# Performance work log

Measured on AMD Instinct MI355X. Metric: run time of the kernel, lower is better.

Reference implementation:

```python
import jax, jax.numpy as jnp
import numpy as np

B = 2
SPATIAL = (480, 360, 32)  # cylindrical grid (rho, phi, z) as in Cylinder3D
N = 400000
C = 32
EPS = 1e-5
NEG_SLOPE = 0.01
OFFSETS = [(d0, d2) for d0 in (-1, 0, 1) for d2 in (-1, 0, 1)]  # kernel (3,1,3)


def setup_inputs() -> dict:
    key = jax.random.key(0)
    k1, k2 = jax.random.split(key)
    # unique active voxel coordinates: sample unique linear indices then decode
    total = B * SPATIAL[0] * SPATIAL[1] * SPATIAL[2]
    rng = np.random.default_rng(0)
    lin = rng.choice(total, size=N, replace=False).astype(np.int64)
    b = lin // (SPATIAL[0] * SPATIAL[1] * SPATIAL[2])
    r = lin % (SPATIAL[0] * SPATIAL[1] * SPATIAL[2])
    c0 = r // (SPATIAL[1] * SPATIAL[2])
    r = r % (SPATIAL[1] * SPATIAL[2])
    c1 = r // SPATIAL[2]
    c2 = r % SPATIAL[2]
    coords = jnp.asarray(np.stack([b, c0, c1, c2], axis=1), dtype=jnp.int32)
    features = jax.random.normal(k1, (N, C), dtype=jnp.float32)
    weight = jax.random.normal(k2, (9, C, C), dtype=jnp.float32) * (1.0 / np.sqrt(9 * C))
    gamma = jnp.ones((C,), dtype=jnp.float32)
    beta = jnp.zeros((C,), dtype=jnp.float32)
    return {"features": features, "coords": coords, "weight": weight,
            "gamma": gamma, "beta": beta}


def _subm_conv(features, coords, weight):
    n = features.shape[0]
    # dense coordinate -> row-index lookup table (rulebook hash)
    lookup = jnp.full((B,) + SPATIAL, -1, dtype=jnp.int32)
    lookup = lookup.at[coords[:, 0], coords[:, 1], coords[:, 2], coords[:, 3]].set(
        jnp.arange(n, dtype=jnp.int32))
    out = jnp.zeros((n, weight.shape[-1]), dtype=features.dtype)
    for k, (d0, d2) in enumerate(OFFSETS):
        n0 = coords[:, 1] + d0
        n2 = coords[:, 3] + d2
        valid = (n0 >= 0) & (n0 < SPATIAL[0]) & (n2 >= 0) & (n2 < SPATIAL[2])
        nbr = lookup[coords[:, 0],
                     jnp.clip(n0, 0, SPATIAL[0] - 1),
                     coords[:, 2],
                     jnp.clip(n2, 0, SPATIAL[2] - 1)]
        nbr = jnp.where(valid, nbr, -1)
        # gather (masked) -> GEMM -> accumulate (scatter to same active sites)
        gathered = jnp.where((nbr >= 0)[:, None],
                             features[jnp.clip(nbr, 0)], 0.0)
        out = out + gathered @ weight[k]
    return out


def reference(features, coords, weight, gamma, beta):
    x = _subm_conv(features, coords, weight)          # [N, C]
    x = jnp.where(x >= 0, x, NEG_SLOPE * x)           # LeakyReLU (before BN per forward)
    mean = jnp.mean(x, axis=0)                        # BatchNorm1d, training mode
    var = jnp.mean((x - mean) ** 2, axis=0)           # biased variance
    y = (x - mean) * jax.lax.rsqrt(var + EPS) * gamma + beta
    return y
```

## Files before the change

### kernel.cpp

```cpp
#include <hip/hip_runtime.h>

#define S0 480
#define S1 360
#define S2 32
#define CH 32
#define EPS 1e-5f
#define SLOPE 0.01f

#define LOOKUP_INTS (2 * S0 * S1 * S2)
#define LOOKUP_BYTES ((size_t)LOOKUP_INTS * 4)

typedef short short8 __attribute__((ext_vector_type(8)));
typedef float f32x16 __attribute__((ext_vector_type(16)));

__device__ __forceinline__ unsigned short f32_to_bf16_rne(float f) {
    union { float f; unsigned int u; } v; v.f = f;
    unsigned int x = v.u;
    unsigned int r = (x + 0x7FFFu + ((x >> 16) & 1u)) >> 16;
    return (unsigned short)r;
}

__global__ __launch_bounds__(256) void scatter_convert_k(
    const float4* __restrict__ features,
    const int4*   __restrict__ coords,
    int*          __restrict__ lookup,
    unsigned short* __restrict__ featb,
    int n)
{
    int i = blockIdx.x * 256 + threadIdx.x;
    if (i >= n) return;
    int4 c = coords[i];
    int lin = ((c.x * S0 + c.y) * S1 + c.z) * S2 + c.w;
    lookup[lin] = i;

    const float4* fr = features + (size_t)i * 8;
    ushort4* fo = (ushort4*)(featb + (size_t)i * CH);
#pragma unroll
    for (int j = 0; j < 8; ++j) {
        float4 f = fr[j];
        ushort4 u;
        u.x = f32_to_bf16_rne(f.x);
        u.y = f32_to_bf16_rne(f.y);
        u.z = f32_to_bf16_rne(f.z);
        u.w = f32_to_bf16_rne(f.w);
        fo[j] = u;
    }
}

__global__ void bfrag_prep_k(const float* __restrict__ weight,
                             short8* __restrict__ bfrag)
{
    int lane = threadIdx.x;
    int half = lane >> 5;
    int col  = lane & 31;
#pragma unroll
    for (int t = 0; t < 9; ++t)
#pragma unroll
        for (int h = 0; h < 2; ++h) {
            short8 fr;
#pragma unroll
            for (int j = 0; j < 8; ++j) {
                int ic = h * 16 + half * 8 + j;
                fr[j] = (short)f32_to_bf16_rne(weight[t * (CH * CH) + ic * CH + col]);
            }
            bfrag[(t * 2 + h) * 64 + lane] = fr;
        }
}

__global__ __launch_bounds__(256) void conv_mfma_k(
    const short*  __restrict__ featb,
    const int4*   __restrict__ coords,
    const int*    __restrict__ lookup,
    const short8* __restrict__ bfrag,
    float*        __restrict__ xout,
    float*        __restrict__ stats,
    int n, int ntile, int nwaves)
{
    int tid  = threadIdx.x;
    int lane = tid & 63;
    int wv   = tid >> 6;
    int half = lane >> 5;
    int col  = lane & 31;

    short8 B[9][2];
#pragma unroll
    for (int t = 0; t < 9; ++t)
#pragma unroll
        for (int h = 0; h < 2; ++h)
            B[t][h] = bfrag[(t * 2 + h) * 64 + lane];

    float s = 0.f, q = 0.f;

    int gw = blockIdx.x * 4 + wv;
    for (int tile = gw; tile < ntile; tile += nwaves) {
        int p = tile * 32 + col;
        int4 c = coords[p];
        int lin = ((c.x * S0 + c.y) * S1 + c.z) * S2 + c.w;
        int nbr[9];
#pragma unroll
        for (int d0 = 0; d0 < 3; ++d0) {
            int n0 = c.y + d0 - 1;
            bool v0 = (n0 >= 0) & (n0 < S0);
#pragma unroll
            for (int d2 = 0; d2 < 3; ++d2) {
                int n2 = c.w + d2 - 1;
                bool v = v0 & (n2 >= 0) & (n2 < S2);
                nbr[d0 * 3 + d2] = v ? lookup[lin + (d0 - 1) * (S1 * S2) + (d2 - 1)] : -1;
            }
        }

        f32x16 acc;
#pragma unroll
        for (int r = 0; r < 16; ++r) acc[r] = 0.f;

#pragma unroll
        for (int t = 0; t < 9; ++t) {
            int nb = nbr[t];
            short8 a0, a1;
            if (nb >= 0) {
                const short* fp = featb + (size_t)nb * CH;
                a0 = *(const short8*)(fp + half * 8);
                a1 = *(const short8*)(fp + 16 + half * 8);
            } else {
#pragma unroll
                for (int j = 0; j < 8; ++j) { a0[j] = 0; a1[j] = 0; }
            }
            acc = __builtin_amdgcn_mfma_f32_32x32x16_bf16(a0, B[t][0], acc, 0, 0, 0);
            acc = __builtin_amdgcn_mfma_f32_32x32x16_bf16(a1, B[t][1], acc, 0, 0, 0);
        }

        bool live = (p < n);
        float* xrow = xout + (size_t)tile * 32 * CH + col;
#pragma unroll
        for (int r = 0; r < 16; ++r) {
            float v = acc[r];
            v = v >= 0.f ? v : SLOPE * v;
            int row = (r & 3) + 8 * (r >> 2) + 4 * half;
            if (live) xrow[row * CH] = v;
            s += v; q += v * v;
        }
    }

    s += __shfl_xor(s, 32);
    q += __shfl_xor(q, 32);

    __shared__ float lsum[4][32];
    __shared__ float lsq[4][32];
    if (lane < 32) { lsum[wv][col] = s; lsq[wv][col] = q; }
    __syncthreads();
    if (tid < 32) {
        float S = lsum[0][tid] + lsum[1][tid] + lsum[2][tid] + lsum[3][tid];
        atomicAdd(&stats[tid], S);
    } else if (tid < 64) {
        int cc = tid - 32;
        float Q = lsq[0][cc] + lsq[1][cc] + lsq[2][cc] + lsq[3][cc];
        atomicAdd(&stats[CH + cc], Q);
    }
}

__global__ __launch_bounds__(256) void bn_apply_k(
    float* __restrict__ x,
    const float* __restrict__ stats,
    const float* __restrict__ gamma,
    const float* __restrict__ beta,
    int n)
{
    int total4 = n * (CH / 4);
    int stride = gridDim.x * blockDim.x;
    int g = blockIdx.x * blockDim.x + threadIdx.x;
    int c4 = g & 7;

    float scale[4], shift[4];
    float rn = 1.0f / (float)n;
#pragma unroll
    for (int j = 0; j < 4; ++j) {
        int oc = c4 * 4 + j;
        float m  = stats[oc] * rn;
        float v  = stats[CH + oc] * rn - m * m;
        float iv = rsqrtf(v + EPS) * gamma[oc];
        scale[j] = iv;
        shift[j] = beta[oc] - m * iv;
    }

    float4* x4 = (float4*)x;
    for (; g < total4; g += stride) {
        float4 v = x4[g];
        v.x = fmaf(v.x, scale[0], shift[0]);
        v.y = fmaf(v.y, scale[1], shift[1]);
        v.z = fmaf(v.z, scale[2], shift[2]);
        v.w = fmaf(v.w, scale[3], shift[3]);
        x4[g] = v;
    }
}

extern "C" void kernel_launch(void* const* d_in, const int* in_sizes, int n_in,
                              void* d_out, int out_size, void* d_ws, size_t ws_size,
                              hipStream_t stream)
{
    const float* features = (const float*)d_in[0];
    const int4*  coords   = (const int4*)d_in[1];
    const float* weight   = (const float*)d_in[2];
    const float* gamma    = (const float*)d_in[3];
    const float* beta     = (const float*)d_in[4];
    float* out = (float*)d_out;

    int n = in_sizes[0] / CH;
    int ntile = (n + 31) / 32;

    unsigned short* featb = (unsigned short*)d_ws;
    size_t featb_bytes = (size_t)n * CH * 2;
    featb_bytes = (featb_bytes + 255) & ~(size_t)255;
    int* lookup = (int*)((char*)d_ws + featb_bytes);
    char* after_lookup = (char*)lookup + LOOKUP_BYTES;
    short8* bfrag = (short8*)after_lookup;
    float* stats = (float*)(after_lookup + 9 * 2 * 64 * sizeof(short8));

    hipMemsetAsync(lookup, 0xFF, LOOKUP_BYTES, stream);
    hipMemsetAsync(stats, 0, 2 * CH * sizeof(float), stream);

    int blocks = (n + 255) / 256;
    scatter_convert_k<<<blocks, 256, 0, stream>>>(
        (const float4*)features, coords, lookup, featb, n);
    bfrag_prep_k<<<1, 64, 0, stream>>>(weight, bfrag);

    int conv_blocks = 1250;
    int nwaves = conv_blocks * 4;
    conv_mfma_k<<<conv_blocks, 256, 0, stream>>>(
        (const short*)featb, coords, lookup, bfrag, out, stats, n, ntile, nwaves);

    bn_apply_k<<<2048, 256, 0, stream>>>(out, stats, gamma, beta, n);
}
```

Measured before the change: 110.5 us.

## Gather fp32 features directly, store bf16 intermediate, replace atomics with partial-sum reduction

```diff
diff --git a/kernel.cpp b/kernel.cpp
--- a/kernel.cpp
+++ b/kernel.cpp
@@ -1,4 +1,5 @@
 #include <hip/hip_runtime.h>
+#include <hip/hip_bf16.h>
 
 #define S0 480
 #define S1 360
@@ -13,37 +14,20 @@
 typedef short short8 __attribute__((ext_vector_type(8)));
 typedef float f32x16 __attribute__((ext_vector_type(16)));
 
-__device__ __forceinline__ unsigned short f32_to_bf16_rne(float f) {
-    union { float f; unsigned int u; } v; v.f = f;
-    unsigned int x = v.u;
-    unsigned int r = (x + 0x7FFFu + ((x >> 16) & 1u)) >> 16;
-    return (unsigned short)r;
-}
-
-__global__ __launch_bounds__(256) void scatter_convert_k(
-    const float4* __restrict__ features,
-    const int4*   __restrict__ coords,
-    int*          __restrict__ lookup,
-    unsigned short* __restrict__ featb,
-    int n)
+__device__ __forceinline__ unsigned short f2b(float f) {
+    union { __hip_bfloat16 b; unsigned short u; } v;
+    v.b = __float2bfloat16(f);
+    return v.u;
+}
+
+__global__ __launch_bounds__(256) void scatter_k(
+    const int4* __restrict__ coords, int* __restrict__ lookup, int n)
 {
     int i = blockIdx.x * 256 + threadIdx.x;
-    if (i >= n) return;
-    int4 c = coords[i];
-    int lin = ((c.x * S0 + c.y) * S1 + c.z) * S2 + c.w;
-    lookup[lin] = i;
-
-    const float4* fr = features + (size_t)i * 8;
-    ushort4* fo = (ushort4*)(featb + (size_t)i * CH);
-#pragma unroll
-    for (int j = 0; j < 8; ++j) {
-        float4 f = fr[j];
-        ushort4 u;
-        u.x = f32_to_bf16_rne(f.x);
-        u.y = f32_to_bf16_rne(f.y);
-        u.z = f32_to_bf16_rne(f.z);
-        u.w = f32_to_bf16_rne(f.w);
-        fo[j] = u;
+    if (i < n) {
+        int4 c = coords[i];
+        int lin = ((c.x * S0 + c.y) * S1 + c.z) * S2 + c.w;
+        lookup[lin] = i;
     }
 }
 
@@ -61,20 +45,20 @@
 #pragma unroll
             for (int j = 0; j < 8; ++j) {
                 int ic = h * 16 + half * 8 + j;
-                fr[j] = (short)f32_to_bf16_rne(weight[t * (CH * CH) + ic * CH + col]);
+                fr[j] = (short)f2b(weight[t * (CH * CH) + ic * CH + col]);
             }
             bfrag[(t * 2 + h) * 64 + lane] = fr;
         }
 }
 
 __global__ __launch_bounds__(256) void conv_mfma_k(
-    const short*  __restrict__ featb,
-    const int4*   __restrict__ coords,
-    const int*    __restrict__ lookup,
+    const float* __restrict__ features,
+    const int4*  __restrict__ coords,
+    const int*   __restrict__ lookup,
     const short8* __restrict__ bfrag,
-    float*        __restrict__ xout,
-    float*        __restrict__ stats,
-    int n, int ntile, int nwaves)
+    unsigned short* __restrict__ xout,
+    float*        __restrict__ stats_part,
+    int n, int ntile)
 {
     int tid  = threadIdx.x;
     int lane = tid & 63;
@@ -84,59 +68,77 @@
 
     short8 B[9][2];
 #pragma unroll
-    for (int t = 0; t < 9; ++t)
-#pragma unroll
-        for (int h = 0; h < 2; ++h)
-            B[t][h] = bfrag[(t * 2 + h) * 64 + lane];
+    for (int t = 0; t < 9; ++t) {
+        B[t][0] = bfrag[(t * 2 + 0) * 64 + lane];
+        B[t][1] = bfrag[(t * 2 + 1) * 64 + lane];
+    }
+
+    int tile = blockIdx.x * 4 + wv;
+    bool tlive = (tile < ntile);
+    int p  = tile * 32 + col;
+    bool live = tlive && (p < n);
+    int pc = live ? p : 0;
+
+    int4 c = coords[pc];
+    int lin = ((c.x * S0 + c.y) * S1 + c.z) * S2 + c.w;
+    int nbr[9];
+#pragma unroll
+    for (int d0 = 0; d0 < 3; ++d0) {
+        int n0 = c.y + d0 - 1;
+        bool v0 = (n0 >= 0) & (n0 < S0) & live;
+#pragma unroll
+        for (int d2 = 0; d2 < 3; ++d2) {
+            int n2 = c.w + d2 - 1;
+            bool v = v0 & (n2 >= 0) & (n2 < S2);
+            nbr[d0 * 3 + d2] = v ? lookup[lin + (d0 - 1) * (S1 * S2) + (d2 - 1)] : -1;
+        }
+    }
+
+    short8 A0[9], A1[9];
+#pragma unroll
+    for (int t = 0; t < 9; ++t) {
+        int nb = nbr[t];
+        if (nb >= 0) {
+            const float4* fp = (const float4*)(features + (size_t)nb * CH);
+            float4 x0 = fp[half * 2 + 0];
+            float4 x1 = fp[half * 2 + 1];
+            float4 y0 = fp[half * 2 + 4];
+            float4 y1 = fp[half * 2 + 5];
+            short8 a0, a1;
+            a0[0] = (short)f2b(x0.x); a0[1] = (short)f2b(x0.y);
+            a0[2] = (short)f2b(x0.z); a0[3] = (short)f2b(x0.w);
+            a0[4] = (short)f2b(x1.x); a0[5] = (short)f2b(x1.y);
+            a0[6] = (short)f2b(x1.z); a0[7] = (short)f2b(x1.w);
+            a1[0] = (short)f2b(y0.x); a1[1] = (short)f2b(y0.y);
+            a1[2] = (short)f2b(y0.z); a1[3] = (short)f2b(y0.w);
+            a1[4] = (short)f2b(y1.x); a1[5] = (short)f2b(y1.y);
+            a1[6] = (short)f2b(y1.z); a1[7] = (short)f2b(y1.w);
+            A0[t] = a0; A1[t] = a1;
+        } else {
+            short8 z;
+#pragma unroll
+            for (int j = 0; j < 8; ++j) z[j] = 0;
+            A0[t] = z; A1[t] = z;
+        }
+    }
+
+    f32x16 acc;
+#pragma unroll
+    for (int r = 0; r < 16; ++r) acc[r] = 0.f;
+#pragma unroll
+    for (int t = 0; t < 9; ++t) {
+        acc = __builtin_amdgcn_mfma_f32_32x32x16_bf16(A0[t], B[t][0], acc, 0, 0, 0);
+        acc = __builtin_amdgcn_mfma_f32_32x32x16_bf16(A1[t], B[t][1], acc, 0, 0, 0);
+    }
 
     float s = 0.f, q = 0.f;
-
-    int gw = blockIdx.x * 4 + wv;
-    for (int tile = gw; tile < ntile; tile += nwaves) {
-        int p = tile * 32 + col;
-        int4 c = coords[p];
-        int lin = ((c.x * S0 + c.y) * S1 + c.z) * S2 + c.w;
-        int nbr[9];
-#pragma unroll
-        for (int d0 = 0; d0 < 3; ++d0) {
-            int n0 = c.y + d0 - 1;
-            bool v0 = (n0 >= 0) & (n0 < S0);
-#pragma unroll
-            for (int d2 = 0; d2 < 3; ++d2) {
-                int n2 = c.w + d2 - 1;
-                bool v = v0 & (n2 >= 0) & (n2 < S2);
-                nbr[d0 * 3 + d2] = v ? lookup[lin + (d0 - 1) * (S1 * S2) + (d2 - 1)] : -1;
-            }
-        }
-
-        f32x16 acc;
-#pragma unroll
-        for (int r = 0; r < 16; ++r) acc[r] = 0.f;
-
-#pragma unroll
-        for (int t = 0; t < 9; ++t) {
-            int nb = nbr[t];
-            short8 a0, a1;
-            if (nb >= 0) {
-                const short* fp = featb + (size_t)nb * CH;
-                a0 = *(const short8*)(fp + half * 8);
-                a1 = *(const short8*)(fp + 16 + half * 8);
-            } else {
-#pragma unroll
-                for (int j = 0; j < 8; ++j) { a0[j] = 0; a1[j] = 0; }
-            }
-            acc = __builtin_amdgcn_mfma_f32_32x32x16_bf16(a0, B[t][0], acc, 0, 0, 0);
-            acc = __builtin_amdgcn_mfma_f32_32x32x16_bf16(a1, B[t][1], acc, 0, 0, 0);
-        }
-
-        bool live = (p < n);
-        float* xrow = xout + (size_t)tile * 32 * CH + col;
-#pragma unroll
-        for (int r = 0; r < 16; ++r) {
-            float v = acc[r];
-            v = v >= 0.f ? v : SLOPE * v;
-            int row = (r & 3) + 8 * (r >> 2) + 4 * half;
-            if (live) xrow[row * CH] = v;
+#pragma unroll
+    for (int r = 0; r < 16; ++r) {
+        float v = acc[r];
+        v = v >= 0.f ? v : SLOPE * v;
+        int row = (r & 3) + 8 * (r >> 2) + 4 * half;
+        if (live) {
+            xout[((size_t)tile * 32 + row) * CH + col] = f2b(v);
             s += v; q += v * v;
         }
     }
@@ -149,47 +151,69 @@
     if (lane < 32) { lsum[wv][col] = s; lsq[wv][col] = q; }
     __syncthreads();
     if (tid < 32) {
-        float S = lsum[0][tid] + lsum[1][tid] + lsum[2][tid] + lsum[3][tid];
-        atomicAdd(&stats[tid], S);
+        stats_part[(size_t)blockIdx.x * 64 + tid] =
+            lsum[0][tid] + lsum[1][tid] + lsum[2][tid] + lsum[3][tid];
     } else if (tid < 64) {
         int cc = tid - 32;
-        float Q = lsq[0][cc] + lsq[1][cc] + lsq[2][cc] + lsq[3][cc];
-        atomicAdd(&stats[CH + cc], Q);
-    }
+        stats_part[(size_t)blockIdx.x * 64 + tid] =
+            lsq[0][cc] + lsq[1][cc] + lsq[2][cc] + lsq[3][cc];
+    }
+}
+
+__global__ __launch_bounds__(256) void reduce_stats_k(
+    const float* __restrict__ part, float* __restrict__ stats, int nb)
+{
+    int c = blockIdx.x;
+    float s = 0.f;
+    for (int i = threadIdx.x; i < nb; i += 256)
+        s += part[(size_t)i * 64 + c];
+#pragma unroll
+    for (int m = 32; m > 0; m >>= 1) s += __shfl_xor(s, m, 64);
+    __shared__ float red[4];
+    int wv = threadIdx.x >> 6;
+    if ((threadIdx.x & 63) == 0) red[wv] = s;
+    __syncthreads();
+    if (threadIdx.x == 0) stats[c] = red[0] + red[1] + red[2] + red[3];
 }
 
 __global__ __launch_bounds__(256) void bn_apply_k(
-    float* __restrict__ x,
+    const unsigned short* __restrict__ xb,
     const float* __restrict__ stats,
     const float* __restrict__ gamma,
     const float* __restrict__ beta,
+    float* __restrict__ out,
     int n)
 {
-    int total4 = n * (CH / 4);
+    int total8 = n * 4;
     int stride = gridDim.x * blockDim.x;
     int g = blockIdx.x * blockDim.x + threadIdx.x;
-    int c4 = g & 7;
-
-    float scale[4], shift[4];
+    int c8 = g & 3;
+
+    float scale[8], shift[8];
     float rn = 1.0f / (float)n;
 #pragma unroll
-    for (int j = 0; j < 4; ++j) {
-        int oc = c4 * 4 + j;
+    for (int j = 0; j < 8; ++j) {
+        int oc = c8 * 8 + j;
         float m  = stats[oc] * rn;
-        float v  = stats[CH + oc] * rn - m * m;
-        float iv = rsqrtf(v + EPS) * gamma[oc];
+        float vv = stats[CH + oc] * rn - m * m;
+        float iv = rsqrtf(vv + EPS) * gamma[oc];
         scale[j] = iv;
         shift[j] = beta[oc] - m * iv;
     }
 
-    float4* x4 = (float4*)x;
-    for (; g < total4; g += stride) {
-        float4 v = x4[g];
-        v.x = fmaf(v.x, scale[0], shift[0]);
-        v.y = fmaf(v.y, scale[1], shift[1]);
-        v.z = fmaf(v.z, scale[2], shift[2]);
-        v.w = fmaf(v.w, scale[3], shift[3]);
-        x4[g] = v;
+    const short8* x8 = (const short8*)xb;
+    float4* o4 = (float4*)out;
+    for (; g < total8; g += stride) {
+        short8 v = x8[g];
+        float f[8];
+#pragma unroll
+        for (int j = 0; j < 8; ++j) {
+            unsigned int u = ((unsigned int)(unsigned short)v[j]) << 16;
+            union { unsigned int u; float f; } w; w.u = u;
+            f[j] = fmaf(w.f, scale[j], shift[j]);
+        }
+        o4[g * 2 + 0] = make_float4(f[0], f[1], f[2], f[3]);
+        o4[g * 2 + 1] = make_float4(f[4], f[5], f[6], f[7]);
     }
 }
 
@@ -206,27 +230,27 @@
 
     int n = in_sizes[0] / CH;
     int ntile = (n + 31) / 32;
-
-    unsigned short* featb = (unsigned short*)d_ws;
-    size_t featb_bytes = (size_t)n * CH * 2;
-    featb_bytes = (featb_bytes + 255) & ~(size_t)255;
-    int* lookup = (int*)((char*)d_ws + featb_bytes);
-    char* after_lookup = (char*)lookup + LOOKUP_BYTES;
-    short8* bfrag = (short8*)after_lookup;
-    float* stats = (float*)(after_lookup + 9 * 2 * 64 * sizeof(short8));
+    int conv_blocks = (ntile + 3) / 4;
+
+    int* lookup = (int*)d_ws;
+    size_t off = LOOKUP_BYTES;
+    unsigned short* xout = (unsigned short*)((char*)d_ws + off);
+    off += (size_t)ntile * 32 * CH * 2;
+    float* stats_part = (float*)((char*)d_ws + off);
+    off += (size_t)conv_blocks * 64 * sizeof(float);
+    short8* bfrag = (short8*)((char*)d_ws + off);
+    off += 9 * 2 * 64 * sizeof(short8);
+    float* stats = (float*)((char*)d_ws + off);
 
     hipMemsetAsync(lookup, 0xFF, LOOKUP_BYTES, stream);
-    hipMemsetAsync(stats, 0, 2 * CH * sizeof(float), stream);
-
-    int blocks = (n + 255) / 256;
-    scatter_convert_k<<<blocks, 256, 0, stream>>>(
-        (const float4*)features, coords, lookup, featb, n);
+
+    scatter_k<<<(n + 255) / 256, 256, 0, stream>>>(coords, lookup, n);
     bfrag_prep_k<<<1, 64, 0, stream>>>(weight, bfrag);
 
-    int conv_blocks = 1250;
-    int nwaves = conv_blocks * 4;
     conv_mfma_k<<<conv_blocks, 256, 0, stream>>>(
-        (const short*)featb, coords, lookup, bfrag, out, stats, n, ntile, nwaves);
-
-    bn_apply_k<<<2048, 256, 0, stream>>>(out, stats, gamma, beta, n);
-}
+        features, coords, lookup, bfrag, xout, stats_part, n, ntile);
+
+    reduce_stats_k<<<64, 256, 0, stream>>>(stats_part, stats, conv_blocks);
+
+    bn_apply_k<<<2048, 256, 0, stream>>>(xout, stats, gamma, beta, out, n);
+}
```

Result: faster. 98.03 us (-11.3%).
